# Kernel optimization log

Measured on AMD Instinct MI355X. Metric: run time of the kernel, lower is better.

## Reference

```python
import jax, jax.numpy as jnp
import numpy as np

B, S, D, H = 2, 2048, 1024, 16
DH = D // H


def setup_inputs() -> dict:
    key = jax.random.key(0)
    ks = jax.random.split(key, 6)
    scale = 0.02
    X = jax.random.normal(ks[0], (B, S, D), dtype=jnp.float32)
    masks = jax.random.randint(ks[1], (B, S), 0, 2).astype(jnp.int32)
    Wq = jax.random.normal(ks[2], (D, D), dtype=jnp.float32) * scale
    Wk = jax.random.normal(ks[3], (D, D), dtype=jnp.float32) * scale
    Wv = jax.random.normal(ks[4], (D, D), dtype=jnp.float32) * scale
    Wo = jax.random.normal(ks[5], (D, D), dtype=jnp.float32) * scale
    return {"X": X, "masks": masks, "Wq": Wq, "Wk": Wk, "Wv": Wv, "Wo": Wo}


def reference(X, masks, Wq, Wk, Wv, Wo):
    b, s, d = X.shape
    masks_b = masks.astype(bool)                       # [B,S] key validity
    lookahead = jnp.triu(jnp.ones((s, s), dtype=bool), 1)  # [S,S] future positions
    pad = ~masks_b[:, None, :]                         # [B,1,S] -> invalid keys
    invalid = pad | lookahead[None, :, :]              # [B,S,S]
    valid = (~invalid)[:, None, :, :].astype(X.dtype)  # [B,1,S,S]

    def split_heads(Y):  # [B,S,D] -> [B,H,S,DH]
        return Y.reshape(b, s, H, DH).transpose(0, 2, 1, 3)

    Q = split_heads(X @ Wq.T)
    K = split_heads(X @ Wk.T)
    V = split_heads(X @ Wv.T)

    Qn = Q / jnp.sqrt(jnp.sum(Q * Q, axis=-1, keepdims=True))
    Kn = K / jnp.sqrt(jnp.sum(K * K, axis=-1, keepdims=True))

    scores = jnp.einsum('bhqd,bhkd->bhqk', Qn, Kn)     # cosine similarities
    att = jax.nn.relu(scores) * valid                  # relu + causal/pad mask
    ctx = jnp.einsum('bhqk,bhkd->bhqd', att, V)
    ctx = ctx * masks_b[:, None, :, None].astype(X.dtype)  # zero padded queries

    out = ctx.transpose(0, 2, 1, 3).reshape(b, s, d)
    return out @ Wo.T
```

## Files before the change

kernel.cpp:

```cpp
#include <hip/hip_runtime.h>
#include <hip/hip_bf16.h>

#define BB 2
#define SS 2048
#define DD 1024
#define HH 16
#define MMR (BB*SS)
#define ND3 3072

typedef __hip_bfloat16 bf;
typedef __bf16 bf16x8 __attribute__((ext_vector_type(8)));
typedef float f32x4 __attribute__((ext_vector_type(4)));
typedef float f32x16 __attribute__((ext_vector_type(16)));

#define VMCNT(n) asm volatile("s_waitcnt vmcnt(" #n ")" ::: "memory")

__device__ __forceinline__ f32x4 mfma16(bf16x8 a, bf16x8 b, f32x4 c) {
    return __builtin_amdgcn_mfma_f32_16x16x32_bf16(a, b, c, 0, 0, 0);
}
__device__ __forceinline__ f32x16 mfma32(bf16x8 a, bf16x8 b, f32x16 c) {
    return __builtin_amdgcn_mfma_f32_32x32x16_bf16(a, b, c, 0, 0, 0);
}
__device__ __forceinline__ unsigned cvt_pk_bf16(float lo, float hi) {
    unsigned r;
    asm("v_cvt_pk_bf16_f32 %0, %1, %2" : "=v"(r) : "v"(lo), "v"(hi));
    return r;
}
__device__ __forceinline__ void pl32swap(unsigned& a, unsigned& b) {
    asm("v_permlane32_swap_b32 %0, %1" : "+v"(a), "+v"(b));
}
__device__ __forceinline__ void glds16(const bf* g, bf* l) {
    __builtin_amdgcn_global_load_lds(
        (const __attribute__((address_space(1))) void*)g,
        (__attribute__((address_space(3))) void*)l,
        16, 0, 0);
}

__global__ __launch_bounds__(256) void k_convert(const float* __restrict__ X,
                                                 const float* __restrict__ Wq,
                                                 const float* __restrict__ Wk,
                                                 const float* __restrict__ Wv,
                                                 const float* __restrict__ Wo,
                                                 bf* __restrict__ Xb,
                                                 bf* __restrict__ Wqkv,
                                                 bf* __restrict__ Wob) {
    const int bid = blockIdx.x;
    const float* src;
    bf* dst;
    int off;
    if (bid < 4096) {
        src = X; dst = Xb; off = bid;
    } else {
        const int r = (bid - 4096) >> 10;
        src = (r == 0) ? Wq : (r == 1) ? Wk : (r == 2) ? Wv : Wo;
        dst = (r < 3) ? (Wqkv + (size_t)r * 1048576) : Wob;
        off = (bid - 4096) & 1023;
    }
    const int j = (off * 256 + threadIdx.x) * 4;
    float4 v = *(const float4*)(src + j);
    bf tmp[4];
    tmp[0] = __float2bfloat16(v.x);
    tmp[1] = __float2bfloat16(v.y);
    tmp[2] = __float2bfloat16(v.z);
    tmp[3] = __float2bfloat16(v.w);
    *(uint2*)(dst + j) = *(const uint2*)tmp;
}

__global__ __launch_bounds__(512, 6) void k_gemm8(const bf* __restrict__ A,
                                                  const bf* __restrict__ Bt,
                                                  const int* __restrict__ masks,
                                                  bf* __restrict__ Qn,
                                                  bf* __restrict__ Kn,
                                                  bf* __restrict__ Vt,
                                                  int nx) {
    constexpr int K = 1024;
    constexpr int T = K >> 5;
    __shared__ __align__(16) bf Asm[3][128 * 32];
    __shared__ __align__(16) bf Bsm[3][128 * 32];
    const int tid = threadIdx.x;
    const int w = tid >> 6, lane = tid & 63, g = lane >> 4, rl = lane & 15;
    const int cpx = gridDim.x >> 3;
    const int swz = (blockIdx.x & 7) * cpx + (blockIdx.x >> 3);
    const int m0 = (swz / nx) * 128, n0 = (swz % nx) * 128;
    const int wr = (w >> 1) * 32, wc = (w & 1) * 64;
    const int lrow = lane >> 2, lseg = lane & 3;
    const int xseg = lseg ^ ((lrow >> 1) & 3);

    f32x4 acc[2][4] = {};

    const bf* asr = A + (size_t)(m0 + w * 16 + lrow) * K + xseg * 8;
    const bf* bsr = Bt + (size_t)(n0 + w * 16 + lrow) * K + xseg * 8;
    bf* const adst = &Asm[0][w * 512];
    bf* const bdst = &Bsm[0][w * 512];

    auto stageP = [&](int buf) {
        glds16(asr, adst + buf * 4096);
        glds16(bsr, bdst + buf * 4096);
        asr += 32; bsr += 32;
    };

    auto computeT = [&](const bf* Ab, const bf* Bb) {
        bf16x8 af[2], bfr[4];
#pragma unroll
        for (int m = 0; m < 2; ++m) {
            const int row = wr + m * 16 + rl;
            af[m] = __builtin_bit_cast(bf16x8,
                *(const int4*)&Ab[row * 32 + (g ^ ((row >> 1) & 3)) * 8]);
        }
#pragma unroll
        for (int n = 0; n < 4; ++n) {
            const int row = wc + n * 16 + rl;
            bfr[n] = __builtin_bit_cast(bf16x8,
                *(const int4*)&Bb[row * 32 + (g ^ ((row >> 1) & 3)) * 8]);
        }
        __builtin_amdgcn_s_setprio(1);
#pragma unroll
        for (int m = 0; m < 2; ++m)
#pragma unroll
            for (int n = 0; n < 4; ++n)
                acc[m][n] = mfma16(af[m], bfr[n], acc[m][n]);
        __builtin_amdgcn_s_setprio(0);
    };

    auto step = [&](auto CURc, auto NXTc, int t) {
        constexpr int CUR = decltype(CURc)::value;
        constexpr int NXT = decltype(NXTc)::value;
        __builtin_amdgcn_sched_barrier(0);
        if (t < T - 1) { VMCNT(2); } else { VMCNT(0); }
        __builtin_amdgcn_s_barrier();
        __builtin_amdgcn_sched_barrier(0);
        if (t + 2 < T) stageP(NXT);
        computeT(&Asm[CUR][0], &Bsm[CUR][0]);
    };
    using c0 = std::integral_constant<int, 0>;
    using c1 = std::integral_constant<int, 1>;
    using c2 = std::integral_constant<int, 2>;

    stageP(0);
    stageP(1);
#pragma unroll 1
    for (int t = 0; t < 30; t += 3) {
        step(c0{}, c2{}, t);
        step(c1{}, c0{}, t + 1);
        step(c2{}, c1{}, t + 2);
    }
    step(c0{}, c2{}, 30);
    step(c1{}, c0{}, 31);

    const int ncol0 = n0 + wc;
    if (ncol0 < 2048) {
        bf* dst = (ncol0 < 1024) ? Qn : Kn;
        const int h2 = (ncol0 >> 6) & 15;
#pragma unroll
        for (int m = 0; m < 2; ++m) {
#pragma unroll
            for (int ri = 0; ri < 4; ++ri) {
                const int row = m0 + wr + m * 16 + g * 4 + ri;
                float ss = 0.f;
#pragma unroll
                for (int n = 0; n < 4; ++n) ss += acc[m][n][ri] * acc[m][n][ri];
#pragma unroll
                for (int d = 1; d < 16; d <<= 1) ss += __shfl_xor(ss, d, 64);
                const float sc = rsqrtf(ss) * (masks[row] ? 1.0f : 0.0f);
                const int b = row >> 11, s = row & 2047;
                const size_t base = ((size_t)(b * HH + h2) * SS + s) * 64;
#pragma unroll
                for (int n = 0; n < 4; ++n)
                    dst[base + n * 16 + rl] = __float2bfloat16(acc[m][n][ri] * sc);
            }
        }
    } else {
        const int h2 = (ncol0 - 2048) >> 6;
        const int b = (m0 + wr) >> 11;
        const int sb = ((m0 + wr) & 2047) + g * 4;
#pragma unroll
        for (int m = 0; m < 2; ++m)
#pragma unroll
            for (int n = 0; n < 4; ++n) {
                const int d = n * 16 + rl;
                bf t4[4];
#pragma unroll
                for (int ri = 0; ri < 4; ++ri) t4[ri] = __float2bfloat16(acc[m][n][ri]);
                *(uint2*)&Vt[((size_t)(b * HH + h2) * 64 + d) * SS + sb + m * 16] =
                    *(uint2*)t4;
            }
    }
}

__global__ __launch_bounds__(256) void k_gemm(const bf* __restrict__ A,
                                              const bf* __restrict__ Bt,
                                              float* __restrict__ Cf,
                                              int nx) {
    constexpr int BM = 64, BN = 128;
    constexpr int K = 1024, N = 1024;
    constexpr int T = K >> 5;
    __shared__ __align__(16) bf Asm[3][BM * 32];
    __shared__ __align__(16) bf Bsm[3][BN * 32];
    const int tid = threadIdx.x;
    const int w = tid >> 6, lane = tid & 63, g = lane >> 4, rl = lane & 15;
    const int cpx = gridDim.x >> 3;
    const int swz = (blockIdx.x & 7) * cpx + (blockIdx.x >> 3);
    const int m0 = (swz / nx) * BM, n0 = (swz % nx) * BN;
    const int wr = (w >> 1) * 32, wc = (w & 1) * 64;
    const int lrow = lane >> 2, lseg = lane & 3;
    const int xseg = lseg ^ ((lrow >> 1) & 3);

    f32x4 acc[2][4] = {};

    const bf* asr = A + (size_t)(m0 + w * 16 + lrow) * K + xseg * 8;
    const bf* bsr = Bt + (size_t)(n0 + w * 16 + lrow) * K + xseg * 8;
    bf* const adst = &Asm[0][w * 512];
    bf* const bdst = &Bsm[0][w * 512];

    auto stageP = [&](int buf) {
        glds16(asr, adst + buf * 2048);
        glds16(bsr, bdst + buf * 4096);
        glds16(bsr + 64 * K, bdst + buf * 4096 + 2048);
        asr += 32; bsr += 32;
    };

    auto computeT = [&](const bf* Ab, const bf* Bb) {
        bf16x8 af[2], bfr[4];
#pragma unroll
        for (int m = 0; m < 2; ++m) {
            const int row = wr + m * 16 + rl;
            af[m] = __builtin_bit_cast(bf16x8,
                *(const int4*)&Ab[row * 32 + (g ^ ((row >> 1) & 3)) * 8]);
        }
#pragma unroll
        for (int n = 0; n < 4; ++n) {
            const int row = wc + n * 16 + rl;
            bfr[n] = __builtin_bit_cast(bf16x8,
                *(const int4*)&Bb[row * 32 + (g ^ ((row >> 1) & 3)) * 8]);
        }
        __builtin_amdgcn_s_setprio(1);
#pragma unroll
        for (int m = 0; m < 2; ++m)
#pragma unroll
            for (int n = 0; n < 4; ++n)
                acc[m][n] = mfma16(af[m], bfr[n], acc[m][n]);
        __builtin_amdgcn_s_setprio(0);
    };

    auto step = [&](auto CURc, auto NXTc, int t) {
        constexpr int CUR = decltype(CURc)::value;
        constexpr int NXT = decltype(NXTc)::value;
        __builtin_amdgcn_sched_barrier(0);
        if (t < T - 1) { VMCNT(3); } else { VMCNT(0); }
        __builtin_amdgcn_s_barrier();
        __builtin_amdgcn_sched_barrier(0);
        if (t + 2 < T) stageP(NXT);
        computeT(&Asm[CUR][0], &Bsm[CUR][0]);
    };
    using c0 = std::integral_constant<int, 0>;
    using c1 = std::integral_constant<int, 1>;
    using c2 = std::integral_constant<int, 2>;

    stageP(0);
    stageP(1);
#pragma unroll 1
    for (int t = 0; t < 30; t += 3) {
        step(c0{}, c2{}, t);
        step(c1{}, c0{}, t + 1);
        step(c2{}, c1{}, t + 2);
    }
    step(c0{}, c2{}, 30);
    step(c1{}, c0{}, 31);

#pragma unroll
    for (int m = 0; m < 2; ++m)
#pragma unroll
        for (int n = 0; n < 4; ++n)
#pragma unroll
            for (int ri = 0; ri < 4; ++ri)
                Cf[(size_t)(m0 + wr + m * 16 + g * 4 + ri) * N + n0 + wc + n * 16 + rl] =
                    acc[m][n][ri];
}

__global__ __launch_bounds__(512) void k_attn(const bf* __restrict__ Qn,
                                              const bf* __restrict__ Kn,
                                              const bf* __restrict__ Vt,
                                              bf* __restrict__ Ctx) {
    __shared__ __align__(16) bf smem[16384];
    bf* const Ksm0 = smem;
    bf* const Vsm0 = smem + 8192;

    const int idx = blockIdx.x;
    const int qt = 15 - (idx >> 5);
    const int by = idx & 31;
    const int b = by >> 4, h = by & 15;
    const int tid = threadIdx.x;
    const int w = tid >> 6, lane = tid & 63;
    const int l31 = lane & 31, hl = lane >> 5;
    const int qh = w >> 1;
    const int kp = w & 1;
    const int qw = qt * 128 + qh * 32;
    const int qg = qw + l31;

    const bf* Qp = Qn + (size_t)by * SS * 64;
    const bf* Kp = Kn + (size_t)by * SS * 64;
    const bf* Vp = Vt + (size_t)by * 64 * SS;

    bf16x8 aqs[4];
#pragma unroll
    for (int st = 0; st < 4; ++st)
        aqs[st] = __builtin_bit_cast(bf16x8,
            *(const int4*)(Qp + (size_t)(qw + l31) * 64 + st * 16 + hl * 8));

    const int srow = lane >> 3;
    const int sblk = (lane & 7) ^ srow;

    const bf* ksr = Kp + (size_t)(w * 8 + srow) * 64 + sblk * 8;
    const bf* vsr = Vp + (size_t)(w * 8 + srow) * SS + sblk * 8;
    bf* const kdst = Ksm0 + w * 512;
    bf* const vdst = Vsm0 + w * 512;

    auto stageP = [&](int buf) {
        glds16(ksr, kdst + buf * 4096);
        glds16(vsr, vdst + buf * 4096);
        ksr += 4096; vsr += 64;
    };

    f32x16 accd[2] = {};

    auto doTile = [&](const bf* Ks, const bf* Vs, int t) {
        const int kb = t * 64 + kp * 32;
        if (kb > qw + 31) return;
        f32x16 pc = {};
        const int r = kp * 32 + l31;
#pragma unroll
        for (int st = 0; st < 4; ++st) {
            bf16x8 ak = __builtin_bit_cast(bf16x8,
                *(const int4*)&Ks[r * 64 + (((2 * st + hl) ^ (r & 7)) << 3)]);
            pc = mfma32(ak, aqs[st], pc);
        }
        const bool dg = (kb + 31 > qw);
        float pv[16];
#pragma unroll
        for (int m2 = 0; m2 < 16; ++m2) {
            float v = fmaxf(pc[m2], 0.0f);
            if (dg) {
                const int kg = kb + (m2 & 3) + 8 * (m2 >> 2) + 4 * hl;
                if (kg > qg) v = 0.0f;
            }
            pv[m2] = v;
        }
        unsigned P[8];
#pragma unroll
        for (int m2 = 0; m2 < 8; ++m2) P[m2] = cvt_pk_bf16(pv[2 * m2], pv[2 * m2 + 1]);
        pl32swap(P[0], P[2]);
        pl32swap(P[1], P[3]);
        pl32swap(P[4], P[6]);
        pl32swap(P[5], P[7]);
#pragma unroll
        for (int s = 0; s < 2; ++s) {
            uint4 pw = {P[4 * s + 0], P[4 * s + 1], P[4 * s + 2], P[4 * s + 3]};
            bf16x8 pa = __builtin_bit_cast(bf16x8, pw);
#pragma unroll
            for (int dt = 0; dt < 2; ++dt) {
                const int d = dt * 32 + l31;
                const int slot = kp * 4 + s * 2 + hl;
                bf16x8 bv = __builtin_bit_cast(bf16x8,
                    *(const int4*)&Vs[d * 64 + ((slot ^ (d & 7)) << 3)]);
                accd[dt] = mfma32(pa, bv, accd[dt]);
            }
        }
    };

    stageP(0);
    __syncthreads();

    const int nt = 2 * qt + 2;
    int t = 0;
    while (t + 1 < nt) {
        stageP(1);
        doTile(Ksm0, Vsm0, t);
        __syncthreads();
        if (t + 2 < nt) stageP(0);
        doTile(Ksm0 + 4096, Vsm0 + 4096, t + 1);
        __syncthreads();
        t += 2;
    }

    float* red = (float*)smem;
    if (kp == 1) {
#pragma unroll
        for (int dt = 0; dt < 2; ++dt)
#pragma unroll
            for (int m2 = 0; m2 < 16; ++m2)
                red[qh * 2048 + (dt * 16 + m2) * 64 + lane] = accd[dt][m2];
    }
    __syncthreads();
    if (kp == 0) {
#pragma unroll
        for (int dt = 0; dt < 2; ++dt)
#pragma unroll
            for (int m2 = 0; m2 < 16; ++m2) {
                const float v = accd[dt][m2] + red[qh * 2048 + (dt * 16 + m2) * 64 + lane];
                const int q = qw + (m2 & 3) + 8 * (m2 >> 2) + 4 * hl;
                const int d = dt * 32 + l31;
                Ctx[(size_t)(b * SS + q) * DD + h * 64 + d] = __float2bfloat16(v);
            }
    }
}

extern "C" void kernel_launch(void* const* d_in, const int* in_sizes, int n_in,
                              void* d_out, int out_size, void* d_ws, size_t ws_size,
                              hipStream_t stream) {
    const float* X  = (const float*)d_in[0];
    const int* masks = (const int*)d_in[1];
    const float* Wq = (const float*)d_in[2];
    const float* Wk = (const float*)d_in[3];
    const float* Wv = (const float*)d_in[4];
    const float* Wo = (const float*)d_in[5];
    float* out = (float*)d_out;
    char* ws = (char*)d_ws;

    const size_t MB = 1024 * 1024;
    bf* Xb   = (bf*)(ws);
    bf* Wqkv = (bf*)(ws + 8  * MB);
    bf* Wob  = (bf*)(ws + 14 * MB);
    bf* Qn   = (bf*)(ws + 16 * MB);
    bf* Kn   = (bf*)(ws + 24 * MB);
    bf* Vt   = (bf*)(ws + 32 * MB);
    bf* Ctx  = (bf*)(ws + 40 * MB);

    k_convert<<<8192, 256, 0, stream>>>(X, Wq, Wk, Wv, Wo, Xb, Wqkv, Wob);

    k_gemm8<<<(ND3 / 128) * (MMR / 128), 512, 0, stream>>>(
        Xb, Wqkv, masks, Qn, Kn, Vt, ND3 / 128);

    k_attn<<<512, 512, 0, stream>>>(Qn, Kn, Vt, Ctx);

    k_gemm<<<(DD / 128) * (MMR / 64), 256, 0, stream>>>(
        Ctx, Wob, out, DD / 128);
}
```

Measured before the change: 93.32 us.

## Switch QKV GEMM to BK=64 double-buffered LDS pipeline with syncthreads

The QKV projection GEMM now stages 64-wide K tiles in a two-buffer LDS scheme instead of 32-wide tiles in a three-buffer ring. Waits are plain __syncthreads rather than explicit vmcnt and s_barrier. This halves the number of K iterations and barriers and uses a new XOR swizzle over 8 segments. In exchange, prefetch depth drops to one tile ahead, and the launch-bounds occupancy hint of 6 is removed. LDS use per block is 64 KiB instead of 48 KiB, which can lower occupancy.

```diff
diff --git a/kernel.cpp b/kernel.cpp
--- a/kernel.cpp
+++ b/kernel.cpp
@@ -66,86 +66,81 @@
     *(uint2*)(dst + j) = *(const uint2*)tmp;
 }
 
-__global__ __launch_bounds__(512, 6) void k_gemm8(const bf* __restrict__ A,
-                                                  const bf* __restrict__ Bt,
-                                                  const int* __restrict__ masks,
-                                                  bf* __restrict__ Qn,
-                                                  bf* __restrict__ Kn,
-                                                  bf* __restrict__ Vt,
-                                                  int nx) {
+__global__ __launch_bounds__(512) void k_gemm8(const bf* __restrict__ A,
+                                               const bf* __restrict__ Bt,
+                                               const int* __restrict__ masks,
+                                               bf* __restrict__ Qn,
+                                               bf* __restrict__ Kn,
+                                               bf* __restrict__ Vt,
+                                               int nx) {
     constexpr int K = 1024;
-    constexpr int T = K >> 5;
-    __shared__ __align__(16) bf Asm[3][128 * 32];
-    __shared__ __align__(16) bf Bsm[3][128 * 32];
+    constexpr int T = K >> 6;
+    __shared__ __align__(16) bf Asm[2][128 * 64];
+    __shared__ __align__(16) bf Bsm[2][128 * 64];
     const int tid = threadIdx.x;
     const int w = tid >> 6, lane = tid & 63, g = lane >> 4, rl = lane & 15;
     const int cpx = gridDim.x >> 3;
     const int swz = (blockIdx.x & 7) * cpx + (blockIdx.x >> 3);
     const int m0 = (swz / nx) * 128, n0 = (swz % nx) * 128;
     const int wr = (w >> 1) * 32, wc = (w & 1) * 64;
-    const int lrow = lane >> 2, lseg = lane & 3;
-    const int xseg = lseg ^ ((lrow >> 1) & 3);
+    const int srow = lane >> 3;
+    const int sblk = (lane & 7) ^ srow;
 
     f32x4 acc[2][4] = {};
 
-    const bf* asr = A + (size_t)(m0 + w * 16 + lrow) * K + xseg * 8;
-    const bf* bsr = Bt + (size_t)(n0 + w * 16 + lrow) * K + xseg * 8;
-    bf* const adst = &Asm[0][w * 512];
-    bf* const bdst = &Bsm[0][w * 512];
+    const bf* asr = A + (size_t)(m0 + w * 16 + srow) * K + sblk * 8;
+    const bf* bsr = Bt + (size_t)(n0 + w * 16 + srow) * K + sblk * 8;
+    bf* const adst = &Asm[0][w * 1024];
+    bf* const bdst = &Bsm[0][w * 1024];
 
     auto stageP = [&](int buf) {
-        glds16(asr, adst + buf * 4096);
-        glds16(bsr, bdst + buf * 4096);
-        asr += 32; bsr += 32;
+        glds16(asr,           adst + buf * 8192);
+        glds16(asr + 8 * K,   adst + buf * 8192 + 512);
+        glds16(bsr,           bdst + buf * 8192);
+        glds16(bsr + 8 * K,   bdst + buf * 8192 + 512);
+        asr += 64; bsr += 64;
     };
 
     auto computeT = [&](const bf* Ab, const bf* Bb) {
-        bf16x8 af[2], bfr[4];
+        bf16x8 af[2][2], bfr[4][2];
 #pragma unroll
         for (int m = 0; m < 2; ++m) {
             const int row = wr + m * 16 + rl;
-            af[m] = __builtin_bit_cast(bf16x8,
-                *(const int4*)&Ab[row * 32 + (g ^ ((row >> 1) & 3)) * 8]);
+#pragma unroll
+            for (int ks = 0; ks < 2; ++ks)
+                af[m][ks] = __builtin_bit_cast(bf16x8,
+                    *(const int4*)&Ab[row * 64 + (((ks * 4 + g) ^ (row & 7)) << 3)]);
         }
 #pragma unroll
         for (int n = 0; n < 4; ++n) {
             const int row = wc + n * 16 + rl;
-            bfr[n] = __builtin_bit_cast(bf16x8,
-                *(const int4*)&Bb[row * 32 + (g ^ ((row >> 1) & 3)) * 8]);
+#pragma unroll
+            for (int ks = 0; ks < 2; ++ks)
+                bfr[n][ks] = __builtin_bit_cast(bf16x8,
+                    *(const int4*)&Bb[row * 64 + (((ks * 4 + g) ^ (row & 7)) << 3)]);
         }
         __builtin_amdgcn_s_setprio(1);
 #pragma unroll
-        for (int m = 0; m < 2; ++m)
-#pragma unroll
-            for (int n = 0; n < 4; ++n)
-                acc[m][n] = mfma16(af[m], bfr[n], acc[m][n]);
+        for (int ks = 0; ks < 2; ++ks)
+#pragma unroll
+            for (int m = 0; m < 2; ++m)
+#pragma unroll
+                for (int n = 0; n < 4; ++n)
+                    acc[m][n] = mfma16(af[m][ks], bfr[n][ks], acc[m][n]);
         __builtin_amdgcn_s_setprio(0);
     };
 
-    auto step = [&](auto CURc, auto NXTc, int t) {
-        constexpr int CUR = decltype(CURc)::value;
-        constexpr int NXT = decltype(NXTc)::value;
-        __builtin_amdgcn_sched_barrier(0);
-        if (t < T - 1) { VMCNT(2); } else { VMCNT(0); }
-        __builtin_amdgcn_s_barrier();
-        __builtin_amdgcn_sched_barrier(0);
-        if (t + 2 < T) stageP(NXT);
-        computeT(&Asm[CUR][0], &Bsm[CUR][0]);
-    };
-    using c0 = std::integral_constant<int, 0>;
-    using c1 = std::integral_constant<int, 1>;
-    using c2 = std::integral_constant<int, 2>;
-
     stageP(0);
-    stageP(1);
+    __syncthreads();
 #pragma unroll 1
-    for (int t = 0; t < 30; t += 3) {
-        step(c0{}, c2{}, t);
-        step(c1{}, c0{}, t + 1);
-        step(c2{}, c1{}, t + 2);
-    }
-    step(c0{}, c2{}, 30);
-    step(c1{}, c0{}, 31);
+    for (int t = 0; t < T; t += 2) {
+        stageP(1);
+        computeT(&Asm[0][0], &Bsm[0][0]);
+        __syncthreads();
+        if (t + 2 < T) stageP(0);
+        computeT(&Asm[1][0], &Bsm[1][0]);
+        __syncthreads();
+    }
 
     const int ncol0 = n0 + wc;
     if (ncol0 < 2048) {
```

After: 96.83 us. 1.04x slower.
